# Optimization experiments

Hardware: AMD Instinct MI355X
Metric: run time of the kernel (lower is better)

Reference implementation:

```python
import jax, jax.numpy as jnp
import numpy as np

HEAD_LENGTH = 4  # hardcoded in original source; scale = 1/sqrt(4) = 0.5
SCALE = 1.0 / HEAD_LENGTH ** 0.5
MASK_FILL = -1.0e9

B, H, S, D = 2, 12, 2048, 64


def setup_inputs() -> dict:
    key = jax.random.key(0)
    kq, kk, kv, km = jax.random.split(key, 4)
    q = jax.random.normal(kq, (B, H, S, D), dtype=jnp.float32)
    k = jax.random.normal(kk, (B, H, S, D), dtype=jnp.float32)
    v = jax.random.normal(kv, (B, H, S, D), dtype=jnp.float32)
    mask = jax.random.randint(km, (B, H, S, S), 0, 2).astype(jnp.bool_)
    return {"q": q, "k": k, "v": v, "mask": mask}


def reference(q, k, v, mask):
    # scores: [B, H, S, S]
    scores = jnp.einsum("bhqd,bhkd->bhqk", q, k) * SCALE
    scores = jnp.where(mask, MASK_FILL, scores)
    attn = jax.nn.softmax(scores, axis=-1)
    # dropout is identity in eval/deterministic mode
    context = jnp.einsum("bhqk,bhkd->bhqd", attn, v)
    return (context, attn)
```

## Files before the change

### kernel.cpp

```cpp
#include <hip/hip_runtime.h>
#include <cstdint>
#include <math.h>

#define S 2048
#define D 64
#define NH 24
#define CTX_ELEMS ((size_t)NH * S * D)
#define SDP_SCALE 0.5f
#define MASK_FILL -1.0e9f
#define PBW 1032

typedef __attribute__((ext_vector_type(8))) short   bf16x8;
typedef __attribute__((ext_vector_type(4))) float   f32x4;

__device__ __forceinline__ unsigned short f2bf(float x) {
    unsigned u = __builtin_bit_cast(unsigned, x);
    u += 0x7FFFu + ((u >> 16) & 1u);
    return (unsigned short)(u >> 16);
}
__device__ __forceinline__ float bf2f(unsigned short b) {
    unsigned u = ((unsigned)b) << 16;
    return __builtin_bit_cast(float, u);
}

__global__ __launch_bounds__(1024, 4) void sdpa_fused(
    const float* __restrict__ q, const float* __restrict__ k,
    const float* __restrict__ v, const int* __restrict__ mask,
    float* __restrict__ out)
{
    const int t    = threadIdx.x;
    const int w    = t >> 6;
    const int lane = t & 63;
    const int quad = lane >> 4, n = lane & 15;
    const int rbase = blockIdx.x * 16;
    const int bh    = rbase >> 11;

    __shared__ unsigned short pb[16 * PBW];
    __shared__ float mwS[16][16];
    __shared__ float lwS[16][16];
    __shared__ float MS[16];
    __shared__ float iLS[16];
    __shared__ float ctxred[16 * D];

    ctxred[t] = 0.f;

    bf16x8 qfh[2], qfl[2];
    #pragma unroll
    for (int ks = 0; ks < 2; ++ks) {
        const float* qp = q + (size_t)(rbase + n) * D + ks * 32 + quad * 8;
        float4 a = *(const float4*)qp;
        float4 b = *(const float4*)(qp + 4);
        float c[8] = {a.x, a.y, a.z, a.w, b.x, b.y, b.z, b.w};
        #pragma unroll
        for (int u = 0; u < 8; ++u) {
            unsigned short hb = f2bf(c[u]);
            qfh[ks][u] = (short)hb;
            qfl[ks][u] = (short)f2bf(c[u] - bf2f(hb));
        }
    }

    const float* khead = k + (size_t)bh * S * D;
    const float* vhead = v + (size_t)bh * S * D;

    float s_reg[8][4];
    float m4[4] = {-INFINITY, -INFINITY, -INFINITY, -INFINITY};
    #pragma unroll
    for (int i = 0; i < 8; ++i) {
        const int tile = w + 16 * i;
        f32x4 c = {0.f, 0.f, 0.f, 0.f};
        #pragma unroll
        for (int ks = 0; ks < 2; ++ks) {
            const float* kp = khead + (size_t)(tile * 16 + n) * D + ks * 32 + quad * 8;
            float4 ka = *(const float4*)kp;
            float4 kb = *(const float4*)(kp + 4);
            float ce[8] = {ka.x, ka.y, ka.z, ka.w, kb.x, kb.y, kb.z, kb.w};
            bf16x8 bh_, bl_;
            #pragma unroll
            for (int u = 0; u < 8; ++u) {
                unsigned short hb = f2bf(ce[u]);
                bh_[u] = (short)hb;
                bl_[u] = (short)f2bf(ce[u] - bf2f(hb));
            }
            c = __builtin_amdgcn_mfma_f32_16x16x32_bf16(qfh[ks], bh_, c, 0, 0, 0);
            c = __builtin_amdgcn_mfma_f32_16x16x32_bf16(qfl[ks], bh_, c, 0, 0, 0);
            c = __builtin_amdgcn_mfma_f32_16x16x32_bf16(qfh[ks], bl_, c, 0, 0, 0);
        }
        const int colb = tile * 16 + n;
        #pragma unroll
        for (int r = 0; r < 4; ++r) {
            float sv = c[r] * SDP_SCALE;
            const int rowg = rbase + quad * 4 + r;
            if (mask[(size_t)rowg * S + colb] != 0) sv = MASK_FILL;
            s_reg[i][r] = sv;
            m4[r] = fmaxf(m4[r], sv);
        }
    }

    #pragma unroll
    for (int r = 0; r < 4; ++r) {
        #pragma unroll
        for (int off = 1; off < 16; off <<= 1)
            m4[r] = fmaxf(m4[r], __shfl_xor(m4[r], off, 64));
    }
    float l4[4] = {0.f, 0.f, 0.f, 0.f};
    #pragma unroll
    for (int i = 0; i < 8; ++i) {
        #pragma unroll
        for (int r = 0; r < 4; ++r)
            l4[r] += __expf(s_reg[i][r] - m4[r]);
    }
    #pragma unroll
    for (int r = 0; r < 4; ++r) {
        #pragma unroll
        for (int off = 1; off < 16; off <<= 1)
            l4[r] += __shfl_xor(l4[r], off, 64);
    }
    if (n == 0) {
        #pragma unroll
        for (int r = 0; r < 4; ++r) {
            mwS[w][quad * 4 + r] = m4[r];
            lwS[w][quad * 4 + r] = l4[r];
        }
    }
    __syncthreads();

    if (t < 16) {
        float M = -INFINITY;
        #pragma unroll
        for (int ww = 0; ww < 16; ++ww) M = fmaxf(M, mwS[ww][t]);
        float L = 0.f;
        #pragma unroll
        for (int ww = 0; ww < 16; ++ww) L += lwS[ww][t] * __expf(mwS[ww][t] - M);
        MS[t]  = M;
        iLS[t] = 1.0f / L;
    }
    __syncthreads();

    float* attn = out + CTX_ELEMS;
    f32x4 acc[4] = {{0.f,0.f,0.f,0.f},{0.f,0.f,0.f,0.f},
                    {0.f,0.f,0.f,0.f},{0.f,0.f,0.f,0.f}};

    #pragma unroll
    for (int h = 0; h < 2; ++h) {
        #pragma unroll
        for (int ii = 0; ii < 4; ++ii) {
            const int i    = h * 4 + ii;
            const int tile = w + 16 * i;
            const int colb = tile * 16 + n;
            const int kloc = colb - h * 1024;
            #pragma unroll
            for (int r = 0; r < 4; ++r) {
                const int row  = quad * 4 + r;
                const int rowg = rbase + row;
                float p = __expf(s_reg[i][r] - MS[row]) * iLS[row];
                attn[(size_t)rowg * S + colb] = p;
                pb[row * PBW + kloc] = f2bf(p);
            }
        }
        __syncthreads();

        #pragma unroll
        for (int ks = 0; ks < 2; ++ks) {
            const int kloc0 = w * 64 + ks * 32 + quad * 8;
            bf16x8 af = *(const bf16x8*)&pb[n * PBW + kloc0];
            const int kg = h * 1024 + kloc0;
            #pragma unroll
            for (int dt = 0; dt < 4; ++dt) {
                const float* vp = vhead + (size_t)kg * D + dt * 16 + n;
                bf16x8 vb;
                #pragma unroll
                for (int j = 0; j < 8; ++j) vb[j] = (short)f2bf(vp[(size_t)j * D]);
                acc[dt] = __builtin_amdgcn_mfma_f32_16x16x32_bf16(af, vb, acc[dt], 0, 0, 0);
            }
        }
        __syncthreads();
    }

    #pragma unroll
    for (int dt = 0; dt < 4; ++dt) {
        #pragma unroll
        for (int r = 0; r < 4; ++r)
            atomicAdd(&ctxred[(quad * 4 + r) * D + dt * 16 + n], acc[dt][r]);
    }
    __syncthreads();

    out[(size_t)(rbase + (t >> 6)) * D + (t & 63)] = ctxred[t];
}

extern "C" void kernel_launch(void* const* d_in, const int* in_sizes, int n_in,
                              void* d_out, int out_size, void* d_ws, size_t ws_size,
                              hipStream_t stream) {
    const float* q    = (const float*)d_in[0];
    const float* k    = (const float*)d_in[1];
    const float* v    = (const float*)d_in[2];
    const int*   mask = (const int*)d_in[3];
    float* out = (float*)d_out;

    sdpa_fused<<<NH * S / 16, 1024, 0, stream>>>(q, k, v, mask, out);
}
```

Before: 1.172 ms.

## Stage mask and V in LDS, coalesce attention stores, split PV across waves

```diff
diff --git a/kernel.cpp b/kernel.cpp
--- a/kernel.cpp
+++ b/kernel.cpp
@@ -8,10 +8,13 @@
 #define CTX_ELEMS ((size_t)NH * S * D)
 #define SDP_SCALE 0.5f
 #define MASK_FILL -1.0e9f
-#define PBW 1032
+
+#define PQW 260
+#define VQW 76
 
 typedef __attribute__((ext_vector_type(8))) short   bf16x8;
 typedef __attribute__((ext_vector_type(4))) float   f32x4;
+typedef __attribute__((ext_vector_type(4))) unsigned short us4;
 
 __device__ __forceinline__ unsigned short f2bf(float x) {
     unsigned u = __builtin_bit_cast(unsigned, x);
@@ -35,7 +38,11 @@
     const int rbase = blockIdx.x * 16;
     const int bh    = rbase >> 11;
 
-    __shared__ unsigned short pb[16 * PBW];
+    __shared__ __align__(16) char pool[16640 + 38912];
+    unsigned char* maskS = (unsigned char*)pool;
+    float*          pq   = (float*)pool;
+    unsigned short* vq   = (unsigned short*)(pool + 16640);
+
     __shared__ float mwS[16][16];
     __shared__ float lwS[16][16];
     __shared__ float MS[16];
@@ -44,6 +51,21 @@
 
     ctxred[t] = 0.f;
 
+    {
+        const int4* m4p = (const int4*)(mask + (size_t)rbase * S);
+        #pragma unroll
+        for (int u = 0; u < 8; ++u) {
+            const int idx = u * 1024 + t;
+            int4 mv = m4p[idx];
+            uchar4 mb;
+            mb.x = (unsigned char)(mv.x != 0);
+            mb.y = (unsigned char)(mv.y != 0);
+            mb.z = (unsigned char)(mv.z != 0);
+            mb.w = (unsigned char)(mv.w != 0);
+            *(uchar4*)&maskS[idx * 4] = mb;
+        }
+    }
+
     bf16x8 qfh[2], qfl[2];
     #pragma unroll
     for (int ks = 0; ks < 2; ++ks) {
@@ -58,6 +80,7 @@
             qfl[ks][u] = (short)f2bf(c[u] - bf2f(hb));
         }
     }
+    __syncthreads();
 
     const float* khead = k + (size_t)bh * S * D;
     const float* vhead = v + (size_t)bh * S * D;
@@ -85,12 +108,10 @@
             c = __builtin_amdgcn_mfma_f32_16x16x32_bf16(qfl[ks], bh_, c, 0, 0, 0);
             c = __builtin_amdgcn_mfma_f32_16x16x32_bf16(qfh[ks], bl_, c, 0, 0, 0);
         }
-        const int colb = tile * 16 + n;
         #pragma unroll
         for (int r = 0; r < 4; ++r) {
             float sv = c[r] * SDP_SCALE;
-            const int rowg = rbase + quad * 4 + r;
-            if (mask[(size_t)rowg * S + colb] != 0) sv = MASK_FILL;
+            if (maskS[(quad * 4 + r) * 2048 + tile * 16 + n]) sv = MASK_FILL;
             s_reg[i][r] = sv;
             m4[r] = fmaxf(m4[r], sv);
         }
@@ -106,8 +127,11 @@
     #pragma unroll
     for (int i = 0; i < 8; ++i) {
         #pragma unroll
-        for (int r = 0; r < 4; ++r)
-            l4[r] += __expf(s_reg[i][r] - m4[r]);
+        for (int r = 0; r < 4; ++r) {
+            float e = __expf(s_reg[i][r] - m4[r]);
+            s_reg[i][r] = e;
+            l4[r] += e;
+        }
     }
     #pragma unroll
     for (int r = 0; r < 4; ++r) {
@@ -136,51 +160,67 @@
     }
     __syncthreads();
 
+    float f4[4];
+    #pragma unroll
+    for (int r = 0; r < 4; ++r)
+        f4[r] = __expf(m4[r] - MS[quad * 4 + r]) * iLS[quad * 4 + r];
+
     float* attn = out + CTX_ELEMS;
-    f32x4 acc[4] = {{0.f,0.f,0.f,0.f},{0.f,0.f,0.f,0.f},
-                    {0.f,0.f,0.f,0.f},{0.f,0.f,0.f,0.f}};
-
-    #pragma unroll
-    for (int h = 0; h < 2; ++h) {
-        #pragma unroll
-        for (int ii = 0; ii < 4; ++ii) {
-            const int i    = h * 4 + ii;
-            const int tile = w + 16 * i;
-            const int colb = tile * 16 + n;
-            const int kloc = colb - h * 1024;
+    const int s_sl = w & 7;
+    const int dt0  = (w >> 3) * 2;
+    f32x4 acc2[2] = {{0.f,0.f,0.f,0.f},{0.f,0.f,0.f,0.f}};
+
+    #pragma unroll
+    for (int ch = 0; ch < 8; ++ch) {
+        {
+            const float4* v4 = (const float4*)(vhead + (size_t)ch * 256 * D);
             #pragma unroll
-            for (int r = 0; r < 4; ++r) {
-                const int row  = quad * 4 + r;
-                const int rowg = rbase + row;
-                float p = __expf(s_reg[i][r] - MS[row]) * iLS[row];
-                attn[(size_t)rowg * S + colb] = p;
-                pb[row * PBW + kloc] = f2bf(p);
+            for (int u = 0; u < 4; ++u) {
+                const int idx = u * 1024 + t;
+                const int kloc = idx >> 4, d0 = (idx & 15) * 4;
+                float4 vv = v4[idx];
+                us4 vb = { f2bf(vv.x), f2bf(vv.y), f2bf(vv.z), f2bf(vv.w) };
+                *(us4*)&vq[kloc * VQW + d0] = vb;
             }
         }
+        #pragma unroll
+        for (int r = 0; r < 4; ++r)
+            pq[(quad * 4 + r) * PQW + w * 16 + n] = s_reg[ch][r] * f4[r];
         __syncthreads();
 
-        #pragma unroll
-        for (int ks = 0; ks < 2; ++ks) {
-            const int kloc0 = w * 64 + ks * 32 + quad * 8;
-            bf16x8 af = *(const bf16x8*)&pb[n * PBW + kloc0];
-            const int kg = h * 1024 + kloc0;
+        {
+            const int row = t >> 6, c4 = (t & 63) * 4;
+            float4 pv = *(const float4*)&pq[row * PQW + c4];
+            *(float4*)(attn + (size_t)(rbase + row) * S + ch * 256 + c4) = pv;
+        }
+
+        bf16x8 af;
+        {
+            const float* ap = &pq[n * PQW + s_sl * 32 + quad * 8];
+            float4 a0 = *(const float4*)ap;
+            float4 a1 = *(const float4*)(ap + 4);
+            af[0] = (short)f2bf(a0.x); af[1] = (short)f2bf(a0.y);
+            af[2] = (short)f2bf(a0.z); af[3] = (short)f2bf(a0.w);
+            af[4] = (short)f2bf(a1.x); af[5] = (short)f2bf(a1.y);
+            af[6] = (short)f2bf(a1.z); af[7] = (short)f2bf(a1.w);
+        }
+        #pragma unroll
+        for (int di = 0; di < 2; ++di) {
+            const int dt = dt0 + di;
+            bf16x8 vb;
             #pragma unroll
-            for (int dt = 0; dt < 4; ++dt) {
-                const float* vp = vhead + (size_t)kg * D + dt * 16 + n;
-                bf16x8 vb;
-                #pragma unroll
-                for (int j = 0; j < 8; ++j) vb[j] = (short)f2bf(vp[(size_t)j * D]);
-                acc[dt] = __builtin_amdgcn_mfma_f32_16x16x32_bf16(af, vb, acc[dt], 0, 0, 0);
-            }
+            for (int j = 0; j < 8; ++j)
+                vb[j] = (short)vq[(s_sl * 32 + quad * 8 + j) * VQW + dt * 16 + n];
+            acc2[di] = __builtin_amdgcn_mfma_f32_16x16x32_bf16(af, vb, acc2[di], 0, 0, 0);
         }
         __syncthreads();
     }
 
     #pragma unroll
-    for (int dt = 0; dt < 4; ++dt) {
+    for (int di = 0; di < 2; ++di) {
         #pragma unroll
         for (int r = 0; r < 4; ++r)
-            atomicAdd(&ctxred[(quad * 4 + r) * D + dt * 16 + n], acc[dt][r]);
+            atomicAdd(&ctxred[(quad * 4 + r) * D + (dt0 + di) * 16 + n], acc2[di][r]);
     }
     __syncthreads();
 
```

Measured after the change: 1.137 ms. 3.0% less time.
